# Kernel optimization log

Measured on AMD Instinct MI355X. Metric: run time of the kernel, lower is better.

## Reference

```python
import jax, jax.numpy as jnp
import numpy as np

EPS = 1e-8

def _unit(v):
    # matches unitization(): v / (||v|| + 1e-8), norm over last (xyz) axis
    return v / (jnp.linalg.norm(v, axis=-1, keepdims=True) + EPS)

def setup_inputs() -> dict:
    key = jax.random.key(0)
    ks = jax.random.split(key, 6)
    B, C, P, S = 16, 76, 1024, 32  # 12 + C_in(=64) channels
    inp = jax.random.normal(ks[0], (B, C, P, S), jnp.float32)
    normal = jax.random.normal(ks[1], (B, P, 3), jnp.float32)
    w1 = jax.random.normal(ks[2], (128, 73), jnp.float32) * 0.1
    b1 = jnp.zeros((128,), jnp.float32)
    w2 = jax.random.normal(ks[3], (128, 128), jnp.float32) * 0.1
    b2 = jnp.zeros((128,), jnp.float32)
    return {"input": inp, "normal": normal, "w1": w1, "b1": b1, "w2": w2, "b2": b2}

def reference(input, normal, w1, b1, w2, b2):
    # channel layout: [0:3]=abs coords, [3:6]=neighbor normals, [6:9]=relative coords,
    # [9:12]=neighbor azimuth dirs, [12:]=input features (C_in=64)
    other_normal = input[:, 3:6]   # (B,3,P,S)
    rel = input[:, 6:9]            # (B,3,P,S)
    other_dir = input[:, 9:12]     # (B,3,P,S)
    feats = input[:, 12:]          # (B,C_in,P,S)

    # azimuth vector: mean of relative coords over neighbors excluding centroid slot
    azi = jnp.mean(rel[:, :, :, 1:], axis=3).transpose(0, 2, 1)  # (B,P,3)

    # PointAlign rotation: local frame with z = unit normal,
    # x = azimuth projected onto tangent plane, y = z x x (row-stacked rotation)
    n = _unit(normal)
    a = _unit(azi)
    xax = _unit(a - jnp.sum(a * n, axis=-1, keepdims=True) * n)
    yax = jnp.cross(n, xax)
    R = jnp.stack([xax, yax, n], axis=2)  # (B,P,3,3)

    def align(v):  # (B,3,P,S) -> (B,3,P,S): rotate each neighbor vector into local frame
        return jnp.einsum('bpij,bjps->bips', R, v)

    azi_u = _unit(azi)                                  # (B,P,3)
    dir_dif = align(azi_u.transpose(0, 2, 1)[:, :, :, None] - other_dir)

    # x[:,0:3] = aligned relative coords, then concat other_normal + dir_difs
    x = jnp.concatenate([align(rel), feats, align(other_normal), dir_dif], axis=1)  # (B,73,P,S)

    # shared MLP: two 1x1 convs + ReLU
    h = jax.nn.relu(jnp.einsum('oc,bcps->bops', w1, x) + b1[None, :, None, None])
    h = jax.nn.relu(jnp.einsum('oc,bcps->bops', w2, h) + b2[None, :, None, None])

    pooled = jnp.max(h, axis=3)  # max_pool2d over nsample -> (B,128,P)
    # not last layer: prepend unit azimuth vector
    return jnp.concatenate([azi_u.transpose(0, 2, 1), pooled], axis=1)  # (B,131,P)
```

## Files before the change

### kernel.cpp

```cpp
#include <hip/hip_runtime.h>
#include <hip/hip_bf16.h>

#define NB 16
#define NP 1024
#define NS 32
#define NC 76
#define XSTR 104
#define HSTR 136
#define TPB 8

typedef __attribute__((ext_vector_type(8))) short bf16x8;
typedef __attribute__((ext_vector_type(4))) float f32x4;

__device__ inline short f2bf(float f) {
  unsigned u = __builtin_bit_cast(unsigned, f);
  u = u + 0x7fffu + ((u >> 16) & 1u);
  return (short)(u >> 16);
}
__device__ inline unsigned cvt_pk_bf16(float lo, float hi) {
  unsigned r;
  asm("v_cvt_pk_bf16_f32 %0, %1, %2" : "=v"(r) : "v"(lo), "v"(hi));
  return r;
}
__device__ inline int swzx(int col, int k) {
  return (col * XSTR + k) ^ (((col >> 4) & 7) << 3);
}
__device__ inline int swzh(int col, int k) {
  return (col * HSTR + k) ^ (((col >> 4) & 7) << 3);
}
__device__ inline float dpp_max16(float v) {
  int x;
  x = __builtin_amdgcn_update_dpp(0, __builtin_bit_cast(int, v), 0xB1, 0xf, 0xf, true);
  v = fmaxf(v, __builtin_bit_cast(float, x));
  x = __builtin_amdgcn_update_dpp(0, __builtin_bit_cast(int, v), 0x4E, 0xf, 0xf, true);
  v = fmaxf(v, __builtin_bit_cast(float, x));
  x = __builtin_amdgcn_update_dpp(0, __builtin_bit_cast(int, v), 0x141, 0xf, 0xf, true);
  v = fmaxf(v, __builtin_bit_cast(float, x));
  x = __builtin_amdgcn_update_dpp(0, __builtin_bit_cast(int, v), 0x140, 0xf, 0xf, true);
  v = fmaxf(v, __builtin_bit_cast(float, x));
  return v;
}

__global__ __launch_bounds__(512, 2)
void mlp_kernel(const float* __restrict__ inp, const float* __restrict__ w1g,
                const float* __restrict__ b1g, const float* __restrict__ w2g,
                const float* __restrict__ b2g, const float* __restrict__ normal,
                float* __restrict__ out) {
  __shared__ short xb[128 * XSTR];
  __shared__ short hb[128 * HSTR];
  const int tid = threadIdx.x;
  const int lane = tid & 63;
  const int wv = tid >> 6;
  const int wr = wv >> 1;
  const int wc = wv & 1;
  const int l15 = lane & 15;
  const int l4 = lane >> 4;

  const int tile0 = blockIdx.x * TPB;

  const int s4  = tid & 7;
  const int flp = (tid >> 3) & 3;
  const int chq = tid >> 5;
  const int colb = flp*32 + 4*s4;

  bf16x8 w1f[2][3];
#pragma unroll
  for (int mf = 0; mf < 2; ++mf)
#pragma unroll
    for (int ks = 0; ks < 3; ++ks) {
      bf16x8 a;
#pragma unroll
      for (int j = 0; j < 8; ++j) {
        int row = 32*wr + 16*mf + l15;
        int kk = 32*ks + 8*l4 + j;
        float v = 0.f;
        if (kk < 73) {
          int c = (kk < 64) ? (kk + 3) : ((kk < 67) ? (kk - 64) : kk);
          v = w1g[row*73 + c];
        } else if (kk == 73) {
          v = b1g[row];
        }
        a[j] = f2bf(v);
      }
      w1f[mf][ks] = a;
    }
  bf16x8 w2f[2][4];
#pragma unroll
  for (int mf = 0; mf < 2; ++mf)
#pragma unroll
    for (int ks = 0; ks < 4; ++ks) {
      bf16x8 a;
#pragma unroll
      for (int j = 0; j < 8; ++j) {
        int row = 32*wr + 16*mf + l15;
        int kk = 32*ks + 8*l4 + j;
        a[j] = f2bf(w2g[row*128 + kk]);
      }
      w2f[mf][ks] = a;
    }
  float bias2[2][4];
#pragma unroll
  for (int mf = 0; mf < 2; ++mf)
#pragma unroll
    for (int r = 0; r < 4; ++r)
      bias2[mf][r] = b2g[32*wr + 16*mf + 4*l4 + r];

  for (int i = tid; i < 128*23; i += 512) {
    int col = i / 23;
    int k = 73 + (i - col*23);
    xb[swzx(col, k)] = (k == 73) ? (short)0x3F80 : (short)0;
  }

  float4 sf0, sf1, sf2, sf3;
  auto stage = [&](int it2) {
    const int tile = tile0 + it2;
    const int bb = tile >> 8;
    const int pb = (tile & 255) * 4;
    const float* base = inp + ((size_t)((bb*NC + 12 + 4*chq)*NP) + pb + flp)*NS + 4*s4;
    sf0 = *(const float4*)(base + 0*(size_t)NP*NS);
    sf1 = *(const float4*)(base + 1*(size_t)NP*NS);
    sf2 = *(const float4*)(base + 2*(size_t)NP*NS);
    sf3 = *(const float4*)(base + 3*(size_t)NP*NS);
  };

  auto fill = [&](int it2) {
    const float* f0 = (const float*)&sf0;
    const float* f1 = (const float*)&sf1;
    const float* f2 = (const float*)&sf2;
    const float* f3 = (const float*)&sf3;
#pragma unroll
    for (int j = 0; j < 4; ++j) {
      uint2 pk;
      pk.x = cvt_pk_bf16(f0[j], f1[j]);
      pk.y = cvt_pk_bf16(f2[j], f3[j]);
      *(uint2*)&xb[swzx(colb + j, 4*chq)] = pk;
    }
    if (tid < 128) {
      const int tile = tile0 + it2;
      const int bb = tile >> 8;
      const int pb = (tile & 255) * 4;
      const int col = tid;
      const int lp = col >> 5, s = col & 31;
      const int p = pb + lp;
      float rel[3], on[3], od[3];
#pragma unroll
      for (int i = 0; i < 3; ++i) {
        rel[i] = inp[(size_t)((bb*NC + 6 + i)*NP + p)*NS + s];
        on[i]  = inp[(size_t)((bb*NC + 3 + i)*NP + p)*NS + s];
        od[i]  = inp[(size_t)((bb*NC + 9 + i)*NP + p)*NS + s];
      }
      float az[3];
#pragma unroll
      for (int i = 0; i < 3; ++i) {
        float sum = rel[i];
#pragma unroll
        for (int m = 1; m < 32; m <<= 1) sum += __shfl_xor(sum, m);
        float v0 = __shfl(rel[i], lane & 32);
        az[i] = (sum - v0) * (1.f/31.f);
      }
      float nr[3];
#pragma unroll
      for (int i = 0; i < 3; ++i) nr[i] = normal[(size_t)(bb*NP + p)*3 + i];
      float nn = sqrtf(nr[0]*nr[0] + nr[1]*nr[1] + nr[2]*nr[2]) + 1e-8f;
      nr[0] /= nn; nr[1] /= nn; nr[2] /= nn;
      float an = sqrtf(az[0]*az[0] + az[1]*az[1] + az[2]*az[2]) + 1e-8f;
      float au[3] = {az[0]/an, az[1]/an, az[2]/an};
      float d = au[0]*nr[0] + au[1]*nr[1] + au[2]*nr[2];
      float xax[3] = {au[0] - d*nr[0], au[1] - d*nr[1], au[2] - d*nr[2]};
      float xn = sqrtf(xax[0]*xax[0] + xax[1]*xax[1] + xax[2]*xax[2]) + 1e-8f;
      xax[0] /= xn; xax[1] /= xn; xax[2] /= xn;
      float yax[3] = {nr[1]*xax[2] - nr[2]*xax[1],
                      nr[2]*xax[0] - nr[0]*xax[2],
                      nr[0]*xax[1] - nr[1]*xax[0]};
      if (s < 3) {
        float o = (s == 0) ? au[0] : ((s == 1) ? au[1] : au[2]);
        out[(size_t)(bb*131 + s)*NP + p] = o;
      }
      float xv[9];
#pragma unroll
      for (int r = 0; r < 3; ++r) {
        const float* Rr = (r == 0) ? xax : ((r == 1) ? yax : nr);
        xv[r]   = Rr[0]*rel[0] + Rr[1]*rel[1] + Rr[2]*rel[2];
        xv[3+r] = Rr[0]*on[0]  + Rr[1]*on[1]  + Rr[2]*on[2];
        xv[6+r] = (Rr[0]*au[0] + Rr[1]*au[1] + Rr[2]*au[2])
                - (Rr[0]*od[0] + Rr[1]*od[1] + Rr[2]*od[2]);
      }
      int4 pk;
      pk.x = (int)cvt_pk_bf16(xv[0], xv[1]);
      pk.y = (int)cvt_pk_bf16(xv[2], xv[3]);
      pk.z = (int)cvt_pk_bf16(xv[4], xv[5]);
      pk.w = (int)cvt_pk_bf16(xv[6], xv[7]);
      *(int4*)&xb[swzx(col, 64)] = pk;
      xb[swzx(col, 72)] = f2bf(xv[8]);
    }
  };

  stage(0);
  fill(0);
  stage(1);
  __syncthreads();

  for (int it = 0; it < TPB; ++it) {
    const int tile = tile0 + it;
    const int bb = tile >> 8;
    const int pb = (tile & 255) * 4;

    f32x4 acc1[2][4];
#pragma unroll
    for (int mf = 0; mf < 2; ++mf)
#pragma unroll
      for (int nf = 0; nf < 4; ++nf) acc1[mf][nf] = f32x4{0.f,0.f,0.f,0.f};
#pragma unroll
    for (int ks = 0; ks < 3; ++ks) {
      bf16x8 bv[4];
#pragma unroll
      for (int nf = 0; nf < 4; ++nf)
        bv[nf] = *(const bf16x8*)&xb[swzx(64*wc + 16*nf + l15, 32*ks + 8*l4)];
#pragma unroll
      for (int mf = 0; mf < 2; ++mf)
#pragma unroll
        for (int nf = 0; nf < 4; ++nf)
          acc1[mf][nf] = __builtin_amdgcn_mfma_f32_16x16x32_bf16(
              w1f[mf][ks], bv[nf], acc1[mf][nf], 0, 0, 0);
    }
#pragma unroll
    for (int mf = 0; mf < 2; ++mf)
#pragma unroll
      for (int nf = 0; nf < 4; ++nf) {
        const int col = 64*wc + 16*nf + l15;
        const int row0 = 32*wr + 16*mf + 4*l4;
        uint2 pk;
        pk.x = cvt_pk_bf16(fmaxf(acc1[mf][nf][0], 0.f), fmaxf(acc1[mf][nf][1], 0.f));
        pk.y = cvt_pk_bf16(fmaxf(acc1[mf][nf][2], 0.f), fmaxf(acc1[mf][nf][3], 0.f));
        *(uint2*)&hb[swzh(col, row0)] = pk;
      }
    __syncthreads();

    if (it + 1 < TPB) fill(it + 1);
    if (it + 2 < TPB) stage(it + 2);

    f32x4 acc2[2][4];
#pragma unroll
    for (int mf = 0; mf < 2; ++mf)
#pragma unroll
      for (int nf = 0; nf < 4; ++nf) acc2[mf][nf] = f32x4{0.f,0.f,0.f,0.f};
#pragma unroll
    for (int ks = 0; ks < 4; ++ks) {
      bf16x8 bv[4];
#pragma unroll
      for (int nf = 0; nf < 4; ++nf)
        bv[nf] = *(const bf16x8*)&hb[swzh(64*wc + 16*nf + l15, 32*ks + 8*l4)];
#pragma unroll
      for (int mf = 0; mf < 2; ++mf)
#pragma unroll
        for (int nf = 0; nf < 4; ++nf)
          acc2[mf][nf] = __builtin_amdgcn_mfma_f32_16x16x32_bf16(
              w2f[mf][ks], bv[nf], acc2[mf][nf], 0, 0, 0);
    }

#pragma unroll
    for (int mf = 0; mf < 2; ++mf)
#pragma unroll
      for (int r = 0; r < 4; ++r) {
        float v0 = fmaxf(acc2[mf][0][r], acc2[mf][1][r]);
        float v1 = fmaxf(acc2[mf][2][r], acc2[mf][3][r]);
        v0 = dpp_max16(v0);
        v1 = dpp_max16(v1);
        v0 = fmaxf(v0 + bias2[mf][r], 0.f);
        v1 = fmaxf(v1 + bias2[mf][r], 0.f);
        if (l15 == 0) {
          const int row = 32*wr + 16*mf + 4*l4 + r;
          *(float2*)&out[(size_t)(bb*131 + 3 + row)*NP + pb + 2*wc] = float2{v0, v1};
        }
      }
    __syncthreads();
  }
}

extern "C" void kernel_launch(void* const* d_in, const int* in_sizes, int n_in,
                              void* d_out, int out_size, void* d_ws, size_t ws_size,
                              hipStream_t stream) {
  const float* inp    = (const float*)d_in[0];
  const float* normal = (const float*)d_in[1];
  const float* w1     = (const float*)d_in[2];
  const float* b1     = (const float*)d_in[3];
  const float* w2     = (const float*)d_in[4];
  const float* b2     = (const float*)d_in[5];
  float* out = (float*)d_out;

  mlp_kernel<<<dim3(NB*NP/4/TPB), dim3(512), 0, stream>>>(
      inp, w1, b1, w2, b2, normal, out);
}
```

Baseline: 69.26 us.

## Halve block tile to two points with 256 threads and prefetch geometry channels

```diff
diff --git a/kernel.cpp b/kernel.cpp
--- a/kernel.cpp
+++ b/kernel.cpp
@@ -23,10 +23,10 @@
   return r;
 }
 __device__ inline int swzx(int col, int k) {
-  return (col * XSTR + k) ^ (((col >> 4) & 7) << 3);
+  return (col * XSTR + k) ^ (((col >> 4) & 3) << 3);
 }
 __device__ inline int swzh(int col, int k) {
-  return (col * HSTR + k) ^ (((col >> 4) & 7) << 3);
+  return (col * HSTR + k) ^ (((col >> 4) & 3) << 3);
 }
 __device__ inline float dpp_max16(float v) {
   int x;
@@ -40,27 +40,37 @@
   v = fmaxf(v, __builtin_bit_cast(float, x));
   return v;
 }
-
-__global__ __launch_bounds__(512, 2)
+__device__ inline float dpp_add16(float v) {
+  int x;
+  x = __builtin_amdgcn_update_dpp(0, __builtin_bit_cast(int, v), 0xB1, 0xf, 0xf, true);
+  v += __builtin_bit_cast(float, x);
+  x = __builtin_amdgcn_update_dpp(0, __builtin_bit_cast(int, v), 0x4E, 0xf, 0xf, true);
+  v += __builtin_bit_cast(float, x);
+  x = __builtin_amdgcn_update_dpp(0, __builtin_bit_cast(int, v), 0x141, 0xf, 0xf, true);
+  v += __builtin_bit_cast(float, x);
+  x = __builtin_amdgcn_update_dpp(0, __builtin_bit_cast(int, v), 0x140, 0xf, 0xf, true);
+  v += __builtin_bit_cast(float, x);
+  return v;
+}
+
+__global__ __launch_bounds__(256, 2)
 void mlp_kernel(const float* __restrict__ inp, const float* __restrict__ w1g,
                 const float* __restrict__ b1g, const float* __restrict__ w2g,
                 const float* __restrict__ b2g, const float* __restrict__ normal,
                 float* __restrict__ out) {
-  __shared__ short xb[128 * XSTR];
-  __shared__ short hb[128 * HSTR];
+  __shared__ short xb[64 * XSTR];
+  __shared__ short hb[64 * HSTR];
   const int tid = threadIdx.x;
   const int lane = tid & 63;
   const int wv = tid >> 6;
-  const int wr = wv >> 1;
-  const int wc = wv & 1;
   const int l15 = lane & 15;
   const int l4 = lane >> 4;
 
   const int tile0 = blockIdx.x * TPB;
 
   const int s4  = tid & 7;
-  const int flp = (tid >> 3) & 3;
-  const int chq = tid >> 5;
+  const int flp = (tid >> 3) & 1;
+  const int chq = tid >> 4;
   const int colb = flp*32 + 4*s4;
 
   bf16x8 w1f[2][3];
@@ -71,7 +81,7 @@
       bf16x8 a;
 #pragma unroll
       for (int j = 0; j < 8; ++j) {
-        int row = 32*wr + 16*mf + l15;
+        int row = 32*wv + 16*mf + l15;
         int kk = 32*ks + 8*l4 + j;
         float v = 0.f;
         if (kk < 73) {
@@ -89,13 +99,12 @@
   for (int mf = 0; mf < 2; ++mf)
 #pragma unroll
     for (int ks = 0; ks < 4; ++ks) {
+      const float* wp = w2g + (size_t)(32*wv + 16*mf + l15)*128 + 32*ks + 8*l4;
+      float4 a0 = *(const float4*)wp;
+      float4 a1 = *(const float4*)(wp + 4);
       bf16x8 a;
-#pragma unroll
-      for (int j = 0; j < 8; ++j) {
-        int row = 32*wr + 16*mf + l15;
-        int kk = 32*ks + 8*l4 + j;
-        a[j] = f2bf(w2g[row*128 + kk]);
-      }
+      a[0] = f2bf(a0.x); a[1] = f2bf(a0.y); a[2] = f2bf(a0.z); a[3] = f2bf(a0.w);
+      a[4] = f2bf(a1.x); a[5] = f2bf(a1.y); a[6] = f2bf(a1.z); a[7] = f2bf(a1.w);
       w2f[mf][ks] = a;
     }
   float bias2[2][4];
@@ -103,27 +112,47 @@
   for (int mf = 0; mf < 2; ++mf)
 #pragma unroll
     for (int r = 0; r < 4; ++r)
-      bias2[mf][r] = b2g[32*wr + 16*mf + 4*l4 + r];
-
-  for (int i = tid; i < 128*23; i += 512) {
+      bias2[mf][r] = b2g[32*wv + 16*mf + 4*l4 + r];
+
+  for (int i = tid; i < 64*23; i += 256) {
     int col = i / 23;
     int k = 73 + (i - col*23);
     xb[swzx(col, k)] = (k == 73) ? (short)0x3F80 : (short)0;
   }
 
   float4 sf0, sf1, sf2, sf3;
+  float sro[9];
   auto stage = [&](int it2) {
     const int tile = tile0 + it2;
-    const int bb = tile >> 8;
-    const int pb = (tile & 255) * 4;
+    const int bb = tile >> 9;
+    const int pb = (tile & 511) * 2;
     const float* base = inp + ((size_t)((bb*NC + 12 + 4*chq)*NP) + pb + flp)*NS + 4*s4;
     sf0 = *(const float4*)(base + 0*(size_t)NP*NS);
     sf1 = *(const float4*)(base + 1*(size_t)NP*NS);
     sf2 = *(const float4*)(base + 2*(size_t)NP*NS);
     sf3 = *(const float4*)(base + 3*(size_t)NP*NS);
+    if (tid < 64) {
+      const int lp = tid >> 5, s = tid & 31;
+      const int p = pb + lp;
+#pragma unroll
+      for (int i = 0; i < 3; ++i) {
+        sro[i]   = inp[(size_t)((bb*NC + 6 + i)*NP + p)*NS + s];
+        sro[3+i] = inp[(size_t)((bb*NC + 3 + i)*NP + p)*NS + s];
+        sro[6+i] = inp[(size_t)((bb*NC + 9 + i)*NP + p)*NS + s];
+      }
+    }
   };
 
   auto fill = [&](int it2) {
+    const int tile = tile0 + it2;
+    const int bb = tile >> 9;
+    const int pb = (tile & 511) * 2;
+    float nr[3];
+    if (tid < 64) {
+      const int p = pb + (tid >> 5);
+#pragma unroll
+      for (int i = 0; i < 3; ++i) nr[i] = normal[(size_t)(bb*NP + p)*3 + i];
+    }
     const float* f0 = (const float*)&sf0;
     const float* f1 = (const float*)&sf1;
     const float* f2 = (const float*)&sf2;
@@ -135,32 +164,18 @@
       pk.y = cvt_pk_bf16(f2[j], f3[j]);
       *(uint2*)&xb[swzx(colb + j, 4*chq)] = pk;
     }
-    if (tid < 128) {
-      const int tile = tile0 + it2;
-      const int bb = tile >> 8;
-      const int pb = (tile & 255) * 4;
+    if (tid < 64) {
       const int col = tid;
-      const int lp = col >> 5, s = col & 31;
-      const int p = pb + lp;
-      float rel[3], on[3], od[3];
+      const int s = col & 31;
+      const int p = pb + (col >> 5);
+      float az[3];
 #pragma unroll
       for (int i = 0; i < 3; ++i) {
-        rel[i] = inp[(size_t)((bb*NC + 6 + i)*NP + p)*NS + s];
-        on[i]  = inp[(size_t)((bb*NC + 3 + i)*NP + p)*NS + s];
-        od[i]  = inp[(size_t)((bb*NC + 9 + i)*NP + p)*NS + s];
-      }
-      float az[3];
-#pragma unroll
-      for (int i = 0; i < 3; ++i) {
-        float sum = rel[i];
-#pragma unroll
-        for (int m = 1; m < 32; m <<= 1) sum += __shfl_xor(sum, m);
-        float v0 = __shfl(rel[i], lane & 32);
+        float sum = dpp_add16(sro[i]);
+        sum += __shfl_xor(sum, 16);
+        float v0 = __shfl(sro[i], lane & 32);
         az[i] = (sum - v0) * (1.f/31.f);
       }
-      float nr[3];
-#pragma unroll
-      for (int i = 0; i < 3; ++i) nr[i] = normal[(size_t)(bb*NP + p)*3 + i];
       float nn = sqrtf(nr[0]*nr[0] + nr[1]*nr[1] + nr[2]*nr[2]) + 1e-8f;
       nr[0] /= nn; nr[1] /= nn; nr[2] /= nn;
       float an = sqrtf(az[0]*az[0] + az[1]*az[1] + az[2]*az[2]) + 1e-8f;
@@ -180,10 +195,10 @@
 #pragma unroll
       for (int r = 0; r < 3; ++r) {
         const float* Rr = (r == 0) ? xax : ((r == 1) ? yax : nr);
-        xv[r]   = Rr[0]*rel[0] + Rr[1]*rel[1] + Rr[2]*rel[2];
-        xv[3+r] = Rr[0]*on[0]  + Rr[1]*on[1]  + Rr[2]*on[2];
+        xv[r]   = Rr[0]*sro[0] + Rr[1]*sro[1] + Rr[2]*sro[2];
+        xv[3+r] = Rr[0]*sro[3] + Rr[1]*sro[4] + Rr[2]*sro[5];
         xv[6+r] = (Rr[0]*au[0] + Rr[1]*au[1] + Rr[2]*au[2])
-                - (Rr[0]*od[0] + Rr[1]*od[1] + Rr[2]*od[2]);
+                - (Rr[0]*sro[6] + Rr[1]*sro[7] + Rr[2]*sro[8]);
       }
       int4 pk;
       pk.x = (int)cvt_pk_bf16(xv[0], xv[1]);
@@ -202,8 +217,8 @@
 
   for (int it = 0; it < TPB; ++it) {
     const int tile = tile0 + it;
-    const int bb = tile >> 8;
-    const int pb = (tile & 255) * 4;
+    const int bb = tile >> 9;
+    const int pb = (tile & 511) * 2;
 
     f32x4 acc1[2][4];
 #pragma unroll
@@ -215,7 +230,7 @@
       bf16x8 bv[4];
 #pragma unroll
       for (int nf = 0; nf < 4; ++nf)
-        bv[nf] = *(const bf16x8*)&xb[swzx(64*wc + 16*nf + l15, 32*ks + 8*l4)];
+        bv[nf] = *(const bf16x8*)&xb[swzx(16*nf + l15, 32*ks + 8*l4)];
 #pragma unroll
       for (int mf = 0; mf < 2; ++mf)
 #pragma unroll
@@ -227,8 +242,8 @@
     for (int mf = 0; mf < 2; ++mf)
 #pragma unroll
       for (int nf = 0; nf < 4; ++nf) {
-        const int col = 64*wc + 16*nf + l15;
-        const int row0 = 32*wr + 16*mf + 4*l4;
+        const int col = 16*nf + l15;
+        const int row0 = 32*wv + 16*mf + 4*l4;
         uint2 pk;
         pk.x = cvt_pk_bf16(fmaxf(acc1[mf][nf][0], 0.f), fmaxf(acc1[mf][nf][1], 0.f));
         pk.y = cvt_pk_bf16(fmaxf(acc1[mf][nf][2], 0.f), fmaxf(acc1[mf][nf][3], 0.f));
@@ -249,7 +264,7 @@
       bf16x8 bv[4];
 #pragma unroll
       for (int nf = 0; nf < 4; ++nf)
-        bv[nf] = *(const bf16x8*)&hb[swzh(64*wc + 16*nf + l15, 32*ks + 8*l4)];
+        bv[nf] = *(const bf16x8*)&hb[swzh(16*nf + l15, 32*ks + 8*l4)];
 #pragma unroll
       for (int mf = 0; mf < 2; ++mf)
 #pragma unroll
@@ -269,8 +284,8 @@
         v0 = fmaxf(v0 + bias2[mf][r], 0.f);
         v1 = fmaxf(v1 + bias2[mf][r], 0.f);
         if (l15 == 0) {
-          const int row = 32*wr + 16*mf + 4*l4 + r;
-          *(float2*)&out[(size_t)(bb*131 + 3 + row)*NP + pb + 2*wc] = float2{v0, v1};
+          const int row = 32*wv + 16*mf + 4*l4 + r;
+          *(float2*)&out[(size_t)(bb*131 + 3 + row)*NP + pb] = float2{v0, v1};
         }
       }
     __syncthreads();
@@ -288,6 +303,6 @@
   const float* b2     = (const float*)d_in[5];
   float* out = (float*)d_out;
 
-  mlp_kernel<<<dim3(NB*NP/4/TPB), dim3(512), 0, stream>>>(
+  mlp_kernel<<<dim3(NB*NP/2/TPB), dim3(256), 0, stream>>>(
       inp, w1, b1, w2, b2, normal, out);
 }
```

After: 71.70 us. 1.04x slower.
